# Performance work log

Measured on AMD Instinct MI355X. Metric: run time of the kernel, lower is better.

The kernel has to match this reference:

```python
import jax, jax.numpy as jnp
import numpy as np

H = 16          # num heads
DH = 64         # head size
D = H * DH      # hidden size 1024
B, S = 2, 2048


def setup_inputs() -> dict:
    key = jax.random.key(0)
    ks = jax.random.split(key, 9)
    scale = 1.0 / np.sqrt(D)
    p = {}
    p["hidden_states"] = jax.random.normal(ks[0], (B, S, D), dtype=jnp.float32)
    for i, name in enumerate(["q", "k", "v", "o"]):
        # stored so that y = x @ W + b (transpose of torch Linear weight)
        p[f"W{name}"] = jax.random.normal(ks[1 + 2 * i], (D, D), dtype=jnp.float32) * scale
        p[f"b{name}"] = jax.random.normal(ks[2 + 2 * i], (D,), dtype=jnp.float32) * 0.01
    return p


def reference(hidden_states, Wq, bq, Wk, bk, Wv, bv, Wo, bo):
    b, s, _ = hidden_states.shape
    q = hidden_states @ Wq + bq  # [B,S,D]
    k = hidden_states @ Wk + bk
    v = hidden_states @ Wv + bv
    # [B,H,S,DH]
    q = q.reshape(b, s, H, DH).transpose(0, 2, 1, 3)
    k = k.reshape(b, s, H, DH).transpose(0, 2, 1, 3)
    v = v.reshape(b, s, H, DH).transpose(0, 2, 1, 3)
    scores = jnp.einsum("bhqd,bhkd->bhqk", q, k) / np.sqrt(DH)
    causal = jnp.triu(jnp.ones((s, s), dtype=bool), k=1)  # True above diagonal -> masked
    scores = jnp.where(causal, -jnp.inf, scores)
    attn = jax.nn.softmax(scores, axis=-1)  # dropout p=0 (eval)
    ctx = jnp.einsum("bhqk,bhkd->bhqd", attn, v)
    ctx = ctx.transpose(0, 2, 1, 3).reshape(b, s, D)
    return ctx @ Wo + bo
```

## Files before the change

### kernel.cpp

```cpp
#include <hip/hip_runtime.h>


typedef _Float16 f16x8 __attribute__((ext_vector_type(8)));
typedef float f32x4 __attribute__((ext_vector_type(4)));

#define GLD_LDS16(g, l)                                                        \
  __builtin_amdgcn_global_load_lds(                                            \
      (__attribute__((address_space(1))) const unsigned int*)(g),              \
      (__attribute__((address_space(3))) unsigned int*)(l), 16, 0, 0)

static constexpr int Sdim = 2048;
static constexpr int Ddim = 1024;
static constexpr int NH = 16;
static constexpr int DH = 64;
static constexpr int Mrows = 4096;
static constexpr int CT = 8;

static constexpr float QSCALE = 0.125f * 1.44269504f;
static constexpr float SHIFT = 4.0f;

struct WtArgs {
  const float *s0, *s1, *s2, *s3;
  _Float16 *d0, *d1, *d2, *d3;
};

__global__ __launch_bounds__(256) void prep(const float* __restrict__ X,
                                            _Float16* __restrict__ Y, WtArgs a) {
  __shared__ _Float16 L[64 * 72];
  const int bid = blockIdx.x, t = threadIdx.x;
  if (bid < 2048) {
    size_t i = ((size_t)bid * 256 + t) * 8;
    float4 f0 = *(const float4*)(X + i);
    float4 f1 = *(const float4*)(X + i + 4);
    alignas(16) _Float16 h[8] = {(_Float16)f0.x, (_Float16)f0.y, (_Float16)f0.z,
                                 (_Float16)f0.w, (_Float16)f1.x, (_Float16)f1.y,
                                 (_Float16)f1.z, (_Float16)f1.w};
    *(uint4*)(Y + i) = *(const uint4*)h;
    return;
  }
  const int w = bid - 2048, z = w >> 8, rem = w & 255;
  const float* src = z == 0 ? a.s0 : z == 1 ? a.s1 : z == 2 ? a.s2 : a.s3;
  _Float16* dst = z == 0 ? a.d0 : z == 1 ? a.d1 : z == 2 ? a.d2 : a.d3;
  const int k0 = (rem & 15) * 64, n0 = (rem >> 4) * 64;
#pragma unroll
  for (int i = 0; i < 4; ++i) {
    int c = i * 256 + t;
    int row = c >> 4, cc = c & 15;
    float4 f = *(const float4*)&src[(size_t)(k0 + row) * Ddim + n0 + cc * 4];
    L[(cc * 4 + 0) * 72 + row] = (_Float16)f.x;
    L[(cc * 4 + 1) * 72 + row] = (_Float16)f.y;
    L[(cc * 4 + 2) * 72 + row] = (_Float16)f.z;
    L[(cc * 4 + 3) * 72 + row] = (_Float16)f.w;
  }
  __syncthreads();
#pragma unroll
  for (int i = 0; i < 2; ++i) {
    int c = i * 256 + t;
    int n = c >> 3, cc = c & 7;
    *(uint4*)&dst[(size_t)(n0 + n) * Ddim + k0 + cc * 8] =
        *(const uint4*)&L[n * 72 + cc * 8];
  }
}

struct GemmArgs {
  const _Float16* A;
  const _Float16 *Bt0, *Bt1, *Bt2;
  const float *b0, *b1, *b2;
  void *o0, *o1, *o2;
};

__global__ __launch_bounds__(256) void gemmQKV(GemmArgs g) {
  constexpr int K = 1024;
  __shared__ _Float16 As[128 * 32];
  __shared__ _Float16 Bs[128 * 32];
  const int z = blockIdx.z;
  const _Float16* A = g.A;
  const _Float16* Bt = z == 0 ? g.Bt0 : z == 1 ? g.Bt1 : g.Bt2;
  const float* bias = z == 0 ? g.b0 : z == 1 ? g.b1 : g.b2;
  void* out = z == 0 ? g.o0 : z == 1 ? g.o1 : g.o2;
  const int m0 = blockIdx.x * 128, n0 = blockIdx.y * 128;
  const int t = threadIdx.x, lane = t & 63, wv = t >> 6;
  const int wm = wv >> 1, wn = wv & 1, quad = lane >> 4, r = lane & 15;

  const int c0 = wv * 64 + lane, c1 = c0 + 256;
  const _Float16* ga0 = A + (size_t)(m0 + (c0 >> 2)) * K + (c0 & 3) * 8;
  const _Float16* ga1 = A + (size_t)(m0 + (c1 >> 2)) * K + (c1 & 3) * 8;
  const _Float16* gb0 = Bt + (size_t)(n0 + (c0 >> 2)) * K + (c0 & 3) * 8;
  const _Float16* gb1 = Bt + (size_t)(n0 + (c1 >> 2)) * K + (c1 & 3) * 8;
  char* lA0 = (char*)As + (wv * 64) * 16;
  char* lA1 = (char*)As + (256 + wv * 64) * 16;
  char* lB0 = (char*)Bs + (wv * 64) * 16;
  char* lB1 = (char*)Bs + (256 + wv * 64) * 16;

  f32x4 acc[4][4] = {};
  for (int kt = 0; kt < K; kt += 32) {
    GLD_LDS16(ga0 + kt, lA0);
    GLD_LDS16(ga1 + kt, lA1);
    GLD_LDS16(gb0 + kt, lB0);
    GLD_LDS16(gb1 + kt, lB1);
    __syncthreads();
    f16x8 af[4], bf[4];
#pragma unroll
    for (int mi = 0; mi < 4; ++mi)
      af[mi] = *(const f16x8*)&As[(wm * 64 + mi * 16 + r) * 32 + quad * 8];
#pragma unroll
    for (int ni = 0; ni < 4; ++ni)
      bf[ni] = *(const f16x8*)&Bs[(wn * 64 + ni * 16 + r) * 32 + quad * 8];
#pragma unroll
    for (int mi = 0; mi < 4; ++mi)
#pragma unroll
      for (int ni = 0; ni < 4; ++ni)
        acc[mi][ni] = __builtin_amdgcn_mfma_f32_16x16x32_f16(af[mi], bf[ni],
                                                             acc[mi][ni], 0, 0, 0);
    __syncthreads();
  }

  const float scale = (z == 0) ? QSCALE : 1.0f;
  float bv[4];
#pragma unroll
  for (int ni = 0; ni < 4; ++ni) bv[ni] = bias[n0 + wn * 64 + ni * 16 + r];
#pragma unroll
  for (int mi = 0; mi < 4; ++mi) {
#pragma unroll
    for (int ni = 0; ni < 4; ++ni) {
      const int n = n0 + wn * 64 + ni * 16 + r;
      if (z == 2) {
        alignas(8) _Float16 h4[4];
#pragma unroll
        for (int reg = 0; reg < 4; ++reg)
          h4[reg] = (_Float16)(acc[mi][ni][reg] + bv[ni]);
        const int m = m0 + wm * 64 + mi * 16 + quad * 4;
        const int b = m >> 11, s = m & 2047, h = n >> 6, dh = n & 63;
        *(uint2*)&((_Float16*)out)[((size_t)(b * NH + h) * DH + dh) * Sdim + s] =
            *(const uint2*)h4;
      } else {
#pragma unroll
        for (int reg = 0; reg < 4; ++reg) {
          const int m = m0 + wm * 64 + mi * 16 + quad * 4 + reg;
          const float v = (acc[mi][ni][reg] + bv[ni]) * scale;
          const int b = m >> 11, s = m & 2047, h = n >> 6, dh = n & 63;
          ((_Float16*)out)[(((size_t)(b * NH + h) * Sdim + s) << 6) + dh] =
              (_Float16)v;
        }
      }
    }
  }
}

__global__ __launch_bounds__(256) void attn(const _Float16* __restrict__ Q,
                                            const _Float16* __restrict__ Kk,
                                            const _Float16* __restrict__ Vt,
                                            float* __restrict__ Ob,
                                            float* __restrict__ Lb) {
  constexpr int LDK = 72;
  __shared__ _Float16 Ks[64 * LDK], Vs[64 * LDK], Ps[4 * 16 * LDK];
  const int id = blockIdx.x, xcd = id & 7, j = id >> 3;
  const int b2 = j / 80, jj = j - 80 * b2;
  int qt, c;
  if (jj < 8) {
    qt = jj; c = 0;
  } else if (jj < 24) {
    qt = 8 + ((jj - 8) >> 1); c = (jj - 8) & 1;
  } else if (jj < 48) {
    qt = 16 + (jj - 24) / 3; c = (jj - 24) % 3;
  } else {
    qt = 24 + ((jj - 48) >> 2); c = (jj - 48) & 3;
  }
  const int bh = xcd + 8 * b2;
  const int t = threadIdx.x, lane = t & 63, wv = t >> 6;
  const int quad = lane >> 4, r = lane & 15;
  const int q0 = qt * 64;
  const int it0 = c * CT;
  const int itn = (it0 + CT < qt + 1) ? it0 + CT : qt + 1;
  const _Float16* Kg = Kk + (size_t)bh * Sdim * DH;
  const _Float16* Vg = Vt + (size_t)bh * DH * Sdim;
  _Float16* Pw = Ps + wv * 16 * LDK;

  const _Float16* Qrow = Q + ((size_t)bh * Sdim + q0 + wv * 16 + r) * DH;
  const f16x8 bq0 = *(const f16x8*)(Qrow + quad * 8);
  const f16x8 bq1 = *(const f16x8*)(Qrow + 32 + quad * 8);

  const int sr0 = t >> 3, sr1 = sr0 + 32, sc0 = (t & 7) * 8;
  const _Float16* pk0 = Kg + (size_t)(it0 * 64 + sr0) * DH + sc0;
  const _Float16* pk1 = Kg + (size_t)(it0 * 64 + sr1) * DH + sc0;
  const _Float16* pv0 = Vg + (size_t)sr0 * Sdim + it0 * 64 + sc0;
  const _Float16* pv1 = Vg + (size_t)sr1 * Sdim + it0 * 64 + sc0;

  float l_i = 0.f;
  f32x4 oacc[4] = {};

  uint4 ka = *(const uint4*)pk0, kb = *(const uint4*)pk1;
  uint4 va = *(const uint4*)pv0, vb = *(const uint4*)pv1;

  for (int it = it0; it < itn; ++it) {
    __syncthreads();
    *(uint4*)&Ks[sr0 * LDK + sc0] = ka;
    *(uint4*)&Ks[sr1 * LDK + sc0] = kb;
    *(uint4*)&Vs[sr0 * LDK + sc0] = va;
    *(uint4*)&Vs[sr1 * LDK + sc0] = vb;
    __syncthreads();
    if (it + 1 < itn) {
      pk0 += 64 * DH; pk1 += 64 * DH; pv0 += 64; pv1 += 64;
      ka = *(const uint4*)pk0; kb = *(const uint4*)pk1;
      va = *(const uint4*)pv0; vb = *(const uint4*)pv1;
    }

    f32x4 sacc[4] = {};
#pragma unroll
    for (int ks = 0; ks < 2; ++ks) {
      const f16x8 bq = ks ? bq1 : bq0;
#pragma unroll
      for (int ni = 0; ni < 4; ++ni) {
        f16x8 ak = *(const f16x8*)&Ks[(ni * 16 + r) * LDK + ks * 32 + quad * 8];
        sacc[ni] =
            __builtin_amdgcn_mfma_f32_16x16x32_f16(ak, bq, sacc[ni], 0, 0, 0);
      }
    }

    if (it == qt) {
      const int qloc = wv * 16 + r;
#pragma unroll
      for (int ni = 0; ni < 4; ++ni)
#pragma unroll
        for (int reg = 0; reg < 4; ++reg)
          if (16 * ni + 4 * quad + reg > qloc) sacc[ni][reg] = -1e30f;
    }
    float lp = 0.f;
#pragma unroll
    for (int ni = 0; ni < 4; ++ni) {
      const float p0 = exp2f(sacc[ni][0] - SHIFT);
      const float p1 = exp2f(sacc[ni][1] - SHIFT);
      const float p2 = exp2f(sacc[ni][2] - SHIFT);
      const float p3 = exp2f(sacc[ni][3] - SHIFT);
      lp += (p0 + p1) + (p2 + p3);
      int2 st;
      st.x = __builtin_bit_cast(int, __builtin_amdgcn_cvt_pkrtz(p0, p1));
      st.y = __builtin_bit_cast(int, __builtin_amdgcn_cvt_pkrtz(p2, p3));
      *(int2*)&Pw[r * LDK + ni * 16 + quad * 4] = st;
    }
    lp += __shfl_xor(lp, 16, 64);
    lp += __shfl_xor(lp, 32, 64);
    l_i += lp;

#pragma unroll
    for (int ks = 0; ks < 2; ++ks) {
      f16x8 ap = *(const f16x8*)&Pw[r * LDK + ks * 32 + quad * 8];
#pragma unroll
      for (int ni = 0; ni < 4; ++ni) {
        f16x8 av = *(const f16x8*)&Vs[(ni * 16 + r) * LDK + ks * 32 + quad * 8];
        oacc[ni] =
            __builtin_amdgcn_mfma_f32_16x16x32_f16(ap, av, oacc[ni], 0, 0, 0);
      }
    }
  }

  const int b = bh >> 4, h = bh & 15;
  if (quad == 0)
    atomicAdd(&Lb[(size_t)bh * Sdim + q0 + wv * 16 + r], l_i);
  float* obase = Ob + ((size_t)b * Sdim + q0 + wv * 16) * Ddim + h * DH;
#pragma unroll
  for (int reg = 0; reg < 4; ++reg)
#pragma unroll
    for (int ni = 0; ni < 4; ++ni)
      atomicAdd(obase + (size_t)(quad * 4 + reg) * Ddim + ni * 16 + r,
                oacc[ni][reg]);
}

__global__ __launch_bounds__(256) void norml(const float* __restrict__ Ob,
                                             const float* __restrict__ Lb,
                                             _Float16* __restrict__ ctx) {
  size_t i = ((size_t)blockIdx.x * 256 + threadIdx.x) * 8;
  const int m = (int)(i >> 10), n = (int)(i & 1023);
  const float rl = 1.0f / Lb[(size_t)(((m >> 11) << 4) + (n >> 6)) * Sdim + (m & 2047)];
  float4 f0 = *(const float4*)(Ob + i);
  float4 f1 = *(const float4*)(Ob + i + 4);
  alignas(16) _Float16 hh[8] = {
      (_Float16)(f0.x * rl), (_Float16)(f0.y * rl), (_Float16)(f0.z * rl),
      (_Float16)(f0.w * rl), (_Float16)(f1.x * rl), (_Float16)(f1.y * rl),
      (_Float16)(f1.z * rl), (_Float16)(f1.w * rl)};
  *(uint4*)(ctx + i) = *(const uint4*)hh;
}

__global__ __launch_bounds__(256) void gemmO(const _Float16* __restrict__ A,
                                             const _Float16* __restrict__ Bt,
                                             const float* __restrict__ bias,
                                             float* __restrict__ out) {
  constexpr int K = 1024;
  __shared__ _Float16 As[64 * 32];
  __shared__ _Float16 Bs[128 * 32];
  const int m0 = blockIdx.x * 64, n0 = blockIdx.y * 128;
  const int t = threadIdx.x, lane = t & 63, wv = t >> 6;
  const int quad = lane >> 4, r = lane & 15;

  const _Float16* ga = A + (size_t)(m0 + (t >> 2)) * K + (t & 3) * 8;
  const int c1 = t + 256;
  const _Float16* gb0 = Bt + (size_t)(n0 + (t >> 2)) * K + (t & 3) * 8;
  const _Float16* gb1 = Bt + (size_t)(n0 + (c1 >> 2)) * K + (c1 & 3) * 8;
  char* lA = (char*)As + t * 16;
  char* lB0 = (char*)Bs + t * 16;
  char* lB1 = (char*)Bs + (256 + t) * 16;

  f32x4 acc[4][2] = {};
  for (int kt = 0; kt < K; kt += 32) {
    GLD_LDS16(ga + kt, lA);
    GLD_LDS16(gb0 + kt, lB0);
    GLD_LDS16(gb1 + kt, lB1);
    __syncthreads();
    f16x8 af[4], bf[2];
#pragma unroll
    for (int mi = 0; mi < 4; ++mi)
      af[mi] = *(const f16x8*)&As[(mi * 16 + r) * 32 + quad * 8];
#pragma unroll
    for (int ni = 0; ni < 2; ++ni)
      bf[ni] = *(const f16x8*)&Bs[(wv * 32 + ni * 16 + r) * 32 + quad * 8];
#pragma unroll
    for (int mi = 0; mi < 4; ++mi)
#pragma unroll
      for (int ni = 0; ni < 2; ++ni)
        acc[mi][ni] = __builtin_amdgcn_mfma_f32_16x16x32_f16(af[mi], bf[ni],
                                                             acc[mi][ni], 0, 0, 0);
    __syncthreads();
  }

  const float bv0 = bias[n0 + wv * 32 + r];
  const float bv1 = bias[n0 + wv * 32 + 16 + r];
#pragma unroll
  for (int mi = 0; mi < 4; ++mi)
#pragma unroll
    for (int reg = 0; reg < 4; ++reg) {
      const int m = m0 + mi * 16 + quad * 4 + reg;
      float* orow = out + (size_t)m * Ddim + n0 + wv * 32 + r;
      orow[0] = acc[mi][0][reg] + bv0;
      orow[16] = acc[mi][1][reg] + bv1;
    }
}

extern "C" void kernel_launch(void* const* d_in, const int* in_sizes, int n_in,
                              void* d_out, int out_size, void* d_ws,
                              size_t ws_size, hipStream_t stream) {
  const float* hid = (const float*)d_in[0];
  const float* Wq = (const float*)d_in[1];
  const float* bq = (const float*)d_in[2];
  const float* Wk = (const float*)d_in[3];
  const float* bk = (const float*)d_in[4];
  const float* Wv = (const float*)d_in[5];
  const float* bv = (const float*)d_in[6];
  const float* Wo = (const float*)d_in[7];
  const float* bo = (const float*)d_in[8];

  char* ws = (char*)d_ws;
  _Float16* Xh = (_Float16*)(ws);
  _Float16* Wqt = (_Float16*)(ws + (8ull << 20));
  _Float16* Wkt = (_Float16*)(ws + (10ull << 20));
  _Float16* Wvt = (_Float16*)(ws + (12ull << 20));
  float* Ob = (float*)(ws);
  _Float16* Qb = (_Float16*)(ws + (16ull << 20));
  _Float16* ctx = (_Float16*)(ws + (16ull << 20));
  _Float16* Kb = (_Float16*)(ws + (24ull << 20));
  _Float16* Vtb = (_Float16*)(ws + (32ull << 20));
  _Float16* Wot = (_Float16*)(ws + (40ull << 20));
  float* Lb = (float*)(ws + (42ull << 20));

  WtArgs wa{Wq, Wk, Wv, Wo, Wqt, Wkt, Wvt, Wot};
  prep<<<dim3(2048 + 1024), 256, 0, stream>>>(hid, Xh, wa);

  GemmArgs g1{Xh, Wqt, Wkt, Wvt, bq, bk, bv, Qb, Kb, Vtb};
  gemmQKV<<<dim3(Mrows / 128, Ddim / 128, 3), 256, 0, stream>>>(g1);

  hipMemsetAsync(Ob, 0, 16ull << 20, stream);
  hipMemsetAsync(Lb, 0, (size_t)32 * Sdim * sizeof(float), stream);

  attn<<<dim3(2560), 256, 0, stream>>>(Qb, Kb, Vtb, Ob, Lb);

  norml<<<dim3(2048), 256, 0, stream>>>(Ob, Lb, ctx);

  gemmO<<<dim3(Mrows / 64, Ddim / 128), 256, 0, stream>>>(ctx, Wot, bo,
                                                          (float*)d_out);
}
```

Before: 209.0 us.

## Restructure attention tiles to load K/V directly into registers and fuse normalization into gemmO

The attention kernel drops the shared-memory staging of K and V. Each wave now covers a 32x32 quadrant of keys by queries, loading K and V fragments straight from global memory into registers. The two key-half waves combine their partial outputs through shared memory before the atomic adds, which halves the number of global atomics. The separate normalization kernel is removed: gemmO reads fp32 Ob, divides by the row sum and converts to fp16 in its A-tile load. This saves a kernel launch and the ctx round trip, at the cost of redundant global loads of K/V per wave and a non-async A load in gemmO.

```diff
diff --git a/kernel.cpp b/kernel.cpp
--- a/kernel.cpp
+++ b/kernel.cpp
@@ -152,10 +152,10 @@
                                             const _Float16* __restrict__ Vt,
                                             float* __restrict__ Ob,
                                             float* __restrict__ Lb) {
-  constexpr int LDK = 72;
-  __shared__ _Float16 Ks[64 * LDK], Vs[64 * LDK], Ps[4 * 16 * LDK];
-  const int id = blockIdx.x, xcd = id & 7, j = id >> 3;
-  const int b2 = j / 80, jj = j - 80 * b2;
+  constexpr int LP = 40;
+  __shared__ char smem[16384];
+  const int id = blockIdx.x, xcd = id & 7, jid = id >> 3;
+  const int b2 = jid / 80, jj = jid - 80 * b2;
   int qt, c;
   if (jj < 8) {
     qt = jj; c = 0;
@@ -168,120 +168,129 @@
   }
   const int bh = xcd + 8 * b2;
   const int t = threadIdx.x, lane = t & 63, wv = t >> 6;
+  const int i = wv & 1, jq = wv >> 1;
   const int quad = lane >> 4, r = lane & 15;
   const int q0 = qt * 64;
   const int it0 = c * CT;
   const int itn = (it0 + CT < qt + 1) ? it0 + CT : qt + 1;
   const _Float16* Kg = Kk + (size_t)bh * Sdim * DH;
   const _Float16* Vg = Vt + (size_t)bh * DH * Sdim;
-  _Float16* Pw = Ps + wv * 16 * LDK;
-
-  const _Float16* Qrow = Q + ((size_t)bh * Sdim + q0 + wv * 16 + r) * DH;
-  const f16x8 bq0 = *(const f16x8*)(Qrow + quad * 8);
-  const f16x8 bq1 = *(const f16x8*)(Qrow + 32 + quad * 8);
-
-  const int sr0 = t >> 3, sr1 = sr0 + 32, sc0 = (t & 7) * 8;
-  const _Float16* pk0 = Kg + (size_t)(it0 * 64 + sr0) * DH + sc0;
-  const _Float16* pk1 = Kg + (size_t)(it0 * 64 + sr1) * DH + sc0;
-  const _Float16* pv0 = Vg + (size_t)sr0 * Sdim + it0 * 64 + sc0;
-  const _Float16* pv1 = Vg + (size_t)sr1 * Sdim + it0 * 64 + sc0;
-
-  float l_i = 0.f;
-  f32x4 oacc[4] = {};
-
-  uint4 ka = *(const uint4*)pk0, kb = *(const uint4*)pk1;
-  uint4 va = *(const uint4*)pv0, vb = *(const uint4*)pv1;
+  _Float16* Pw = (_Float16*)(smem + wv * 2560);
+
+  const _Float16* Qbase = Q + ((size_t)bh * Sdim + q0 + jq * 32 + r) * DH;
+  f16x8 qf[2][2];
+  qf[0][0] = *(const f16x8*)(Qbase + quad * 8);
+  qf[0][1] = *(const f16x8*)(Qbase + 32 + quad * 8);
+  qf[1][0] = *(const f16x8*)(Qbase + 16 * DH + quad * 8);
+  qf[1][1] = *(const f16x8*)(Qbase + 16 * DH + 32 + quad * 8);
+
+  const _Float16* kbase = Kg + (size_t)(it0 * 64 + i * 32 + r) * DH + quad * 8;
+  const _Float16* vbase = Vg + (size_t)r * Sdim + it0 * 64 + i * 32 + quad * 8;
+
+  float l2[2] = {0.f, 0.f};
+  f32x4 oacc[2][4] = {};
 
   for (int it = it0; it < itn; ++it) {
-    __syncthreads();
-    *(uint4*)&Ks[sr0 * LDK + sc0] = ka;
-    *(uint4*)&Ks[sr1 * LDK + sc0] = kb;
-    *(uint4*)&Vs[sr0 * LDK + sc0] = va;
-    *(uint4*)&Vs[sr1 * LDK + sc0] = vb;
-    __syncthreads();
-    if (it + 1 < itn) {
-      pk0 += 64 * DH; pk1 += 64 * DH; pv0 += 64; pv1 += 64;
-      ka = *(const uint4*)pk0; kb = *(const uint4*)pk1;
-      va = *(const uint4*)pv0; vb = *(const uint4*)pv1;
-    }
-
-    f32x4 sacc[4] = {};
-#pragma unroll
-    for (int ks = 0; ks < 2; ++ks) {
-      const f16x8 bq = ks ? bq1 : bq0;
+    f16x8 kf[2][2], vf[4];
+    kf[0][0] = *(const f16x8*)(kbase);
+    kf[0][1] = *(const f16x8*)(kbase + 32);
+    kf[1][0] = *(const f16x8*)(kbase + 16 * DH);
+    kf[1][1] = *(const f16x8*)(kbase + 16 * DH + 32);
+    vf[0] = *(const f16x8*)(vbase);
+    vf[1] = *(const f16x8*)(vbase + 16 * Sdim);
+    vf[2] = *(const f16x8*)(vbase + 32 * Sdim);
+    vf[3] = *(const f16x8*)(vbase + 48 * Sdim);
+    kbase += 64 * DH;
+    vbase += 64;
+
+    f32x4 sacc[2][2] = {};
+#pragma unroll
+    for (int ks = 0; ks < 2; ++ks)
+#pragma unroll
+      for (int mi = 0; mi < 2; ++mi)
+#pragma unroll
+        for (int ni = 0; ni < 2; ++ni)
+          sacc[mi][ni] = __builtin_amdgcn_mfma_f32_16x16x32_f16(
+              kf[mi][ks], qf[ni][ks], sacc[mi][ni], 0, 0, 0);
+
+    if (it == qt) {
+#pragma unroll
+      for (int mi = 0; mi < 2; ++mi)
+#pragma unroll
+        for (int ni = 0; ni < 2; ++ni)
+#pragma unroll
+          for (int reg = 0; reg < 4; ++reg)
+            if (i * 32 + mi * 16 + quad * 4 + reg > jq * 32 + ni * 16 + r)
+              sacc[mi][ni][reg] = -1e30f;
+    }
+
+    float lp[2] = {0.f, 0.f};
+#pragma unroll
+    for (int mi = 0; mi < 2; ++mi)
+#pragma unroll
+      for (int ni = 0; ni < 2; ++ni) {
+        const float p0 = exp2f(sacc[mi][ni][0] - SHIFT);
+        const float p1 = exp2f(sacc[mi][ni][1] - SHIFT);
+        const float p2 = exp2f(sacc[mi][ni][2] - SHIFT);
+        const float p3 = exp2f(sacc[mi][ni][3] - SHIFT);
+        lp[ni] += (p0 + p1) + (p2 + p3);
+        int2 st;
+        st.x = __builtin_bit_cast(int, __builtin_amdgcn_cvt_pkrtz(p0, p1));
+        st.y = __builtin_bit_cast(int, __builtin_amdgcn_cvt_pkrtz(p2, p3));
+        *(int2*)&Pw[(ni * 16 + r) * LP + mi * 16 + quad * 4] = st;
+      }
+#pragma unroll
+    for (int ni = 0; ni < 2; ++ni) {
+      float s = lp[ni];
+      s += __shfl_xor(s, 16, 64);
+      s += __shfl_xor(s, 32, 64);
+      l2[ni] += s;
+    }
+
+#pragma unroll
+    for (int mi = 0; mi < 2; ++mi) {
+      const f16x8 ap = *(const f16x8*)&Pw[(mi * 16 + r) * LP + quad * 8];
+#pragma unroll
+      for (int ni = 0; ni < 4; ++ni)
+        oacc[mi][ni] = __builtin_amdgcn_mfma_f32_16x16x32_f16(ap, vf[ni],
+                                                              oacc[mi][ni], 0, 0, 0);
+    }
+  }
+
+  if (quad == 0) {
+#pragma unroll
+    for (int ni = 0; ni < 2; ++ni)
+      atomicAdd(&Lb[(size_t)bh * Sdim + q0 + jq * 32 + ni * 16 + r], l2[ni]);
+  }
+
+  float* Oex = (float*)smem + jq * 2048;
+  __syncthreads();
+  if (i == 1) {
+#pragma unroll
+    for (int mi = 0; mi < 2; ++mi)
+#pragma unroll
+      for (int ni = 0; ni < 4; ++ni)
+        *(f32x4*)&Oex[(mi * 4 + ni) * 256 + lane * 4] = oacc[mi][ni];
+  }
+  __syncthreads();
+  if (i == 0) {
+    const int b = bh >> 4, h = bh & 15;
+    float* obase = Ob + ((size_t)b * Sdim + q0 + jq * 32) * Ddim + h * DH;
+#pragma unroll
+    for (int mi = 0; mi < 2; ++mi)
 #pragma unroll
       for (int ni = 0; ni < 4; ++ni) {
-        f16x8 ak = *(const f16x8*)&Ks[(ni * 16 + r) * LDK + ks * 32 + quad * 8];
-        sacc[ni] =
-            __builtin_amdgcn_mfma_f32_16x16x32_f16(ak, bq, sacc[ni], 0, 0, 0);
+        const f32x4 other = *(const f32x4*)&Oex[(mi * 4 + ni) * 256 + lane * 4];
+#pragma unroll
+        for (int reg = 0; reg < 4; ++reg)
+          atomicAdd(obase + (size_t)(mi * 16 + quad * 4 + reg) * Ddim + ni * 16 + r,
+                    oacc[mi][ni][reg] + other[reg]);
       }
-    }
-
-    if (it == qt) {
-      const int qloc = wv * 16 + r;
-#pragma unroll
-      for (int ni = 0; ni < 4; ++ni)
-#pragma unroll
-        for (int reg = 0; reg < 4; ++reg)
-          if (16 * ni + 4 * quad + reg > qloc) sacc[ni][reg] = -1e30f;
-    }
-    float lp = 0.f;
-#pragma unroll
-    for (int ni = 0; ni < 4; ++ni) {
-      const float p0 = exp2f(sacc[ni][0] - SHIFT);
-      const float p1 = exp2f(sacc[ni][1] - SHIFT);
-      const float p2 = exp2f(sacc[ni][2] - SHIFT);
-      const float p3 = exp2f(sacc[ni][3] - SHIFT);
-      lp += (p0 + p1) + (p2 + p3);
-      int2 st;
-      st.x = __builtin_bit_cast(int, __builtin_amdgcn_cvt_pkrtz(p0, p1));
-      st.y = __builtin_bit_cast(int, __builtin_amdgcn_cvt_pkrtz(p2, p3));
-      *(int2*)&Pw[r * LDK + ni * 16 + quad * 4] = st;
-    }
-    lp += __shfl_xor(lp, 16, 64);
-    lp += __shfl_xor(lp, 32, 64);
-    l_i += lp;
-
-#pragma unroll
-    for (int ks = 0; ks < 2; ++ks) {
-      f16x8 ap = *(const f16x8*)&Pw[r * LDK + ks * 32 + quad * 8];
-#pragma unroll
-      for (int ni = 0; ni < 4; ++ni) {
-        f16x8 av = *(const f16x8*)&Vs[(ni * 16 + r) * LDK + ks * 32 + quad * 8];
-        oacc[ni] =
-            __builtin_amdgcn_mfma_f32_16x16x32_f16(ap, av, oacc[ni], 0, 0, 0);
-      }
-    }
-  }
-
-  const int b = bh >> 4, h = bh & 15;
-  if (quad == 0)
-    atomicAdd(&Lb[(size_t)bh * Sdim + q0 + wv * 16 + r], l_i);
-  float* obase = Ob + ((size_t)b * Sdim + q0 + wv * 16) * Ddim + h * DH;
-#pragma unroll
-  for (int reg = 0; reg < 4; ++reg)
-#pragma unroll
-    for (int ni = 0; ni < 4; ++ni)
-      atomicAdd(obase + (size_t)(quad * 4 + reg) * Ddim + ni * 16 + r,
-                oacc[ni][reg]);
-}
-
-__global__ __launch_bounds__(256) void norml(const float* __restrict__ Ob,
+  }
+}
+
+__global__ __launch_bounds__(256) void gemmO(const float* __restrict__ Ob,
                                              const float* __restrict__ Lb,
-                                             _Float16* __restrict__ ctx) {
-  size_t i = ((size_t)blockIdx.x * 256 + threadIdx.x) * 8;
-  const int m = (int)(i >> 10), n = (int)(i & 1023);
-  const float rl = 1.0f / Lb[(size_t)(((m >> 11) << 4) + (n >> 6)) * Sdim + (m & 2047)];
-  float4 f0 = *(const float4*)(Ob + i);
-  float4 f1 = *(const float4*)(Ob + i + 4);
-  alignas(16) _Float16 hh[8] = {
-      (_Float16)(f0.x * rl), (_Float16)(f0.y * rl), (_Float16)(f0.z * rl),
-      (_Float16)(f0.w * rl), (_Float16)(f1.x * rl), (_Float16)(f1.y * rl),
-      (_Float16)(f1.z * rl), (_Float16)(f1.w * rl)};
-  *(uint4*)(ctx + i) = *(const uint4*)hh;
-}
-
-__global__ __launch_bounds__(256) void gemmO(const _Float16* __restrict__ A,
                                              const _Float16* __restrict__ Bt,
                                              const float* __restrict__ bias,
                                              float* __restrict__ out) {
@@ -292,19 +301,30 @@
   const int t = threadIdx.x, lane = t & 63, wv = t >> 6;
   const int quad = lane >> 4, r = lane & 15;
 
-  const _Float16* ga = A + (size_t)(m0 + (t >> 2)) * K + (t & 3) * 8;
+  const int arow = m0 + (t >> 2), koff = (t & 3) * 8;
+  const int ab = arow >> 11, as = arow & 2047;
+  const float* ga = Ob + (size_t)arow * K + koff;
+  const float* lrow = Lb + (size_t)(ab * NH) * Sdim + as;
   const int c1 = t + 256;
   const _Float16* gb0 = Bt + (size_t)(n0 + (t >> 2)) * K + (t & 3) * 8;
   const _Float16* gb1 = Bt + (size_t)(n0 + (c1 >> 2)) * K + (c1 & 3) * 8;
-  char* lA = (char*)As + t * 16;
   char* lB0 = (char*)Bs + t * 16;
   char* lB1 = (char*)Bs + (256 + t) * 16;
 
   f32x4 acc[4][2] = {};
   for (int kt = 0; kt < K; kt += 32) {
-    GLD_LDS16(ga + kt, lA);
     GLD_LDS16(gb0 + kt, lB0);
     GLD_LDS16(gb1 + kt, lB1);
+    const int h = (kt + koff) >> 6;
+    const float rl = 1.0f / lrow[(size_t)h * Sdim];
+    float4 f0 = *(const float4*)(ga + kt);
+    float4 f1 = *(const float4*)(ga + kt + 4);
+    int4 ah;
+    ah.x = __builtin_bit_cast(int, __builtin_amdgcn_cvt_pkrtz(f0.x * rl, f0.y * rl));
+    ah.y = __builtin_bit_cast(int, __builtin_amdgcn_cvt_pkrtz(f0.z * rl, f0.w * rl));
+    ah.z = __builtin_bit_cast(int, __builtin_amdgcn_cvt_pkrtz(f1.x * rl, f1.y * rl));
+    ah.w = __builtin_bit_cast(int, __builtin_amdgcn_cvt_pkrtz(f1.z * rl, f1.w * rl));
+    *(int4*)((char*)As + t * 16) = ah;
     __syncthreads();
     f16x8 af[4], bf[2];
 #pragma unroll
@@ -355,7 +375,6 @@
   _Float16* Wvt = (_Float16*)(ws + (12ull << 20));
   float* Ob = (float*)(ws);
   _Float16* Qb = (_Float16*)(ws + (16ull << 20));
-  _Float16* ctx = (_Float16*)(ws + (16ull << 20));
   _Float16* Kb = (_Float16*)(ws + (24ull << 20));
   _Float16* Vtb = (_Float16*)(ws + (32ull << 20));
   _Float16* Wot = (_Float16*)(ws + (40ull << 20));
@@ -372,8 +391,6 @@
 
   attn<<<dim3(2560), 256, 0, stream>>>(Qb, Kb, Vtb, Ob, Lb);
 
-  norml<<<dim3(2048), 256, 0, stream>>>(Ob, Lb, ctx);
-
-  gemmO<<<dim3(Mrows / 64, Ddim / 128), 256, 0, stream>>>(ctx, Wot, bo,
+  gemmO<<<dim3(Mrows / 64, Ddim / 128), 256, 0, stream>>>(Ob, Lb, Wot, bo,
                                                           (float*)d_out);
 }
```

Measured after the change: 239.4 us. 14.5% more time.
